# Performance work log

Measured on AMD Instinct MI355X. Metric: run time of the kernel, lower is better.

The kernel has to match this reference:

```python
import jax, jax.numpy as jnp
import numpy as np

V = 59      # input features (mimic_59f)
H = 128     # hidden size
B = 2048
T = 96

def _uniform(key, shape, fan_in):
    s = 1.0 / np.sqrt(fan_in)
    return jax.random.uniform(key, shape, jnp.float32, -s, s)

def setup_inputs() -> dict:
    key = jax.random.key(0)
    ks = jax.random.split(key, 20)
    x = jax.random.normal(ks[0], (B, T, V), jnp.float32)
    mask = (jax.random.uniform(ks[1], (B, T, V)) < 0.8).astype(jnp.float32)
    deltas = jax.random.uniform(ks[2], (B, T, V), jnp.float32)
    return {
        'x': x, 'mask': mask, 'deltas': deltas,
        # temp_decay_h: Decay(V -> H)
        'Wdh': _uniform(ks[3], (H, V), V), 'bdh': _uniform(ks[4], (H,), V),
        # temp_decay_x: Decay(V -> V, diag)
        'Wdx': _uniform(ks[5], (V, V), V), 'bdx': _uniform(ks[6], (V,), V),
        # hist: Linear(H -> V)
        'Wh': _uniform(ks[7], (V, H), H), 'bh': _uniform(ks[8], (V,), H),
        'Wf': _uniform(ks[9], (V, V), V), 'bf': _uniform(ks[10], (V,), V),
        # weight_combine: Linear(2V -> V)
        'Wc': _uniform(ks[11], (V, 2 * V), 2 * V), 'bc': _uniform(ks[12], (V,), 2 * V),
        # GRUCell(2V -> H): gates ordered [r, z, n]
        'Wih': _uniform(ks[13], (3 * H, 2 * V), 2 * V), 'Whh': _uniform(ks[14], (3 * H, H), H),
        'bih': _uniform(ks[15], (3 * H,), H), 'bhh': _uniform(ks[16], (3 * H,), H),
    }


def reference(x, mask, deltas, Wdh, bdh, Wdx, bdx, Wh, bh, Wf, bf, Wc, bc, Wih, Whh, bih, bhh):
    Bb, Tt, Vv = x.shape
    eye = jnp.eye(Vv, dtype=x.dtype)
    Wdx_d = Wdx * eye            # diagonal decay
    Wf_m = Wf * (1.0 - eye)

    def step(h, inp):
        x_t, m_t, d_t = inp                                  # each [B, V]
        gamma_h = jnp.exp(-jax.nn.relu(d_t @ Wdh.T + bdh))   # [B, H]
        h = h * gamma_h
        x_h = h @ Wh.T + bh                                   # [B, V]
        x_r = m_t * x_t + (1.0 - m_t) * x_h
        xu = x_r @ Wf_m.T + bf
        gamma_x = jnp.exp(-jax.nn.relu(d_t @ Wdx_d.T + bdx))
        beta = jnp.concatenate([gamma_x, m_t], axis=1) @ Wc.T + bc
        x_comb = beta * xu + (1.0 - beta) * x_h
        loss_t = jnp.sum(jnp.abs(x_t - x_comb) * m_t) / (jnp.sum(m_t) + 1e-5)
        x_imp_t = m_t * x_t + (1.0 - m_t) * x_comb
        inp_t = jnp.concatenate([x_imp_t, m_t], axis=1)       # [B, 2V]
        gi = inp_t @ Wih.T + bih                              # [B, 3H]
        gh = h @ Whh.T + bhh
        ir, iz, inn = jnp.split(gi, 3, axis=1)
        hr, hz, hn = jnp.split(gh, 3, axis=1)
        r = jax.nn.sigmoid(ir + hr)
        z = jax.nn.sigmoid(iz + hz)
        n = jnp.tanh(inn + r * hn)
        h_new = (1.0 - z) * n + z * h
        return h_new, (x_imp_t, h_new, loss_t)

    xs = (jnp.swapaxes(x, 0, 1), jnp.swapaxes(mask, 0, 1), jnp.swapaxes(deltas, 0, 1))
    h0 = jnp.zeros((Bb, Wdh.shape[0]), x.dtype)
    _, (x_imp, Hiddens, losses) = jax.lax.scan(step, h0, xs)
    return (jnp.swapaxes(x_imp, 0, 1),      # imputation [B, T, V]
            jnp.sum(losses),                 # xloss scalar
            jnp.swapaxes(Hiddens, 0, 1))     # hidden_state [B, T, H]
```

## Files before the change

kernel.cpp:

```cpp
#include <hip/hip_runtime.h>
#include <hip/hip_bf16.h>
#include <math.h>

#define VF 59
#define HF 128
#define BB 2048
#define TT 96
#define MR 16
#define NBLK (BB / MR)
#define NTH 512

typedef __attribute__((ext_vector_type(8))) short short8;
typedef __attribute__((ext_vector_type(4))) float f32x4;

#define MFMA(a, b, c) __builtin_amdgcn_mfma_f32_16x16x32_bf16((a), (b), (c), 0, 0, 0)

#define WF_INV   0
#define WF_ACC   96
#define WF_DWDX  192
#define WF_END   256
#define U_B1  (WF_END * 2)
#define U_B2  (U_B1 + 8192)
#define U_B3  (U_B2 + 8192)
#define U_B4  (U_B3 + 4096)
#define U_B5  (U_B4 + 8192)
#define U_B6  (U_B5 + 49152)

#define LOSS_IDX (BB * TT * VF)
#define OFF_HID  (BB * TT * VF + 1)

#define S_AD    0
#define S_AH    1024
#define S_AGM   3072
#define S_AIM0  5120
#define S_AIM1  7168
#define S_AXR   9216
#define F_SX    5120
#define F_SM    6080
#define F_SB    7040
#define F_RED   8064
#define F_IDT   8072
#define F_TOT   8168

__device__ __forceinline__ ushort f2bf(float f) {
    __hip_bfloat16 h = __float2bfloat16(f);
    return *reinterpret_cast<ushort*>(&h);
}
__device__ __forceinline__ float sigm(float v) { return 1.f / (1.f + __expf(-v)); }
__device__ __forceinline__ float tanh_f(float v) {
    float c = fminf(fmaxf(v, -15.f), 15.f);
    float e = __expf(-2.f * c);
    return (1.f - e) / (1.f + e);
}
__device__ __forceinline__ int fragIdx(int row, int col) {
    return ((col >> 5) * 64 + ((col >> 3) & 3) * 16 + row) * 8 + (col & 7);
}
__device__ __forceinline__ int betaIdx(int m, int col) {
    return m * 64 + ((col + 4 * m) & 63);
}

__device__ __forceinline__ void block_sync() {
    asm volatile("s_waitcnt lgkmcnt(0)" ::: "memory");
    __builtin_amdgcn_s_barrier();
    asm volatile("" ::: "memory");
}

__global__ __launch_bounds__(128) void prep_zero(float* __restrict__ ws, float* __restrict__ loss_ptr) {
    int tid = threadIdx.x;
    if (tid < TT) ws[WF_ACC + tid] = 0.f;
    if (tid == 96) loss_ptr[0] = 0.f;
}

#define PA_R 128
__global__ __launch_bounds__(256) void prep_acc(const float* __restrict__ mask, float* __restrict__ ws) {
    __shared__ float buf[PA_R * VF];
    __shared__ float acc[TT];
    int tid = threadIdx.x;
    if (tid < TT) acc[tid] = 0.f;
    const float4* src = (const float4*)(mask + (size_t)blockIdx.x * (PA_R * VF));
    float4* dst = (float4*)buf;
    #pragma unroll
    for (int i = 0; i < 8; ++i) {
        int idx = tid + i * 256;
        if (idx < PA_R * VF / 4) dst[idx] = src[idx];
    }
    __syncthreads();
    if (tid < PA_R) {
        float s = 0.f;
        #pragma unroll
        for (int v = 0; v < VF; ++v) s += buf[tid * VF + v];
        int t = (blockIdx.x * PA_R + tid) % TT;
        atomicAdd(&acc[t], s);
    }
    __syncthreads();
    if (tid < TT) atomicAdd(&ws[WF_ACC + tid], acc[tid]);
}

__device__ void packB(const float* __restrict__ W, int G, int K, int tiles, int KS,
                      int zdiag, ushort* __restrict__ dst, int gtid, int gstride) {
    int total = tiles * KS * 512;
    for (int idx = gtid; idx < total; idx += gstride) {
        int j  = idx & 7;
        int l  = (idx >> 3) & 63;
        int tk = idx >> 9;
        int ks = tk % KS;
        int tile = tk / KS;
        int g = tile * 16 + (l & 15);
        int k = ks * 32 + ((l >> 4) << 3) + j;
        float v = 0.f;
        if (g < G && k < K) v = W[g * K + k];
        if (zdiag && g == k) v = 0.f;
        dst[idx] = f2bf(v);
    }
}

__global__ __launch_bounds__(256) void prep_pack(
    const float* __restrict__ Wdh, const float* __restrict__ Wdx,
    const float* __restrict__ Wh,  const float* __restrict__ Wf,
    const float* __restrict__ Wc,  const float* __restrict__ Wih,
    const float* __restrict__ Whh, float* __restrict__ ws)
{
    int blk = blockIdx.x, tid = threadIdx.x;
    if (blk == 64) {
        if (tid < TT) ws[WF_INV + tid] = 1.f / (ws[WF_ACC + tid] + 1e-5f);
        if (tid < VF) ws[WF_DWDX + tid] = Wdx[tid * VF + tid];
        return;
    }
    ushort* wsu = (ushort*)ws;
    int gtid = blk * 256 + tid;
    int gstride = 64 * 256;
    packB(Wdh, HF,     VF,     8,  2, 0, wsu + U_B1, gtid, gstride);
    packB(Wh,  VF,     HF,     4,  4, 0, wsu + U_B2, gtid, gstride);
    packB(Wf,  VF,     VF,     4,  2, 1, wsu + U_B3, gtid, gstride);
    packB(Wc,  VF,     2*VF,   4,  4, 0, wsu + U_B4, gtid, gstride);
    packB(Wih, 3*HF,   2*VF,   24, 4, 0, wsu + U_B5, gtid, gstride);
    packB(Whh, 3*HF,   HF,     24, 4, 0, wsu + U_B6, gtid, gstride);
}

__global__ __launch_bounds__(NTH, 2) void rits_main(
    const float* __restrict__ x, const float* __restrict__ mask, const float* __restrict__ deltas,
    const float* __restrict__ bdh, const float* __restrict__ bdx, const float* __restrict__ bh,
    const float* __restrict__ bf,  const float* __restrict__ bc,
    const float* __restrict__ bih, const float* __restrict__ bhh,
    const float* __restrict__ ws, float* __restrict__ out)
{
    __shared__ __align__(16) float smf[F_TOT];
    ushort* smu = (ushort*)smf;

    const int tid  = threadIdx.x;
    const int lane = tid & 63;
    const int w    = tid >> 6;
    const int ln15 = lane & 15;
    const int quad = lane >> 4;
    const int b0   = blockIdx.x * MR;

    const ushort* wsu = (const ushort*)ws;
    const short8* B1 = (const short8*)(wsu + U_B1);
    const short8* B2 = (const short8*)(wsu + U_B2);
    const short8* B3 = (const short8*)(wsu + U_B3);
    const short8* B4 = (const short8*)(wsu + U_B4);
    const short8* B5 = (const short8*)(wsu + U_B5);
    const short8* B6 = (const short8*)(wsu + U_B6);

    short8 wB1[2];
    #pragma unroll
    for (int i = 0; i < 2; ++i) wB1[i] = B1[(w * 2 + i) * 64 + lane];
    short8 wB24[4];
    #pragma unroll
    for (int ks = 0; ks < 4; ++ks)
        wB24[ks] = (w < 4) ? B2[(w * 4 + ks) * 64 + lane]
                           : B4[((w - 4) * 4 + ks) * 64 + lane];
    short8 wB3[2];
    #pragma unroll
    for (int i = 0; i < 2; ++i) wB3[i] = B3[(((w < 4) ? w : (w - 4)) * 2 + i) * 64 + lane];
    short8 wB5[12], wB6[12];
    #pragma unroll
    for (int tt = 0; tt < 3; ++tt)
        #pragma unroll
        for (int ks = 0; ks < 4; ++ks) {
            wB5[tt * 4 + ks] = B5[((w + tt * 8) * 4 + ks) * 64 + lane];
            wB6[tt * 4 + ks] = B6[((w + tt * 8) * 4 + ks) * 64 + lane];
        }

    const int jH = w * 16 + ln15;
    const float c_bdh = bdh[jH];
    const float c_br  = bih[jH]       + bhh[jH];
    const float c_bz  = bih[jH + 128] + bhh[jH + 128];
    const float c_bin = bih[jH + 256];
    const float c_bhn = bhh[jH + 256];
    const int vC = (w < 4 ? w : w - 4) * 16 + ln15;
    const float c_bh = (vC < VF) ? bh[vC] : 0.f;
    const float c_bf = (vC < VF) ? bf[vC] : 0.f;
    const float c_bc = (vC < VF) ? bc[vC] : 0.f;

    const int q  = tid & 255;
    const int lr = q >> 4;
    const int lc = q & 15;
    const size_t rowbase = (size_t)(b0 + lr) * (TT * VF);
    const float* px = x + rowbase;
    const float* pm = mask + rowbase;
    const float* pd = deltas + rowbase;
    float wdx4[4], bdx4[4];
    #pragma unroll
    for (int k = 0; k < 4; ++k) {
        int v = lc + 16 * k;
        wdx4[k] = (v < VF) ? ws[WF_DWDX + v] : 0.f;
        bdx4[k] = (v < VF) ? bdx[v] : 0.f;
    }

    float hreg[4] = {0.f, 0.f, 0.f, 0.f};

    for (int i = tid; i < F_TOT; i += NTH) smf[i] = 0.f;
    __syncthreads();

    if (tid < TT) smf[F_IDT + tid] = ws[WF_INV + tid];
    if (w >= 4) {
        #pragma unroll
        for (int k = 0; k < 4; ++k) {
            int v = lc + 16 * k;
            if (v < VF) {
                float xv = px[v], mv = pm[v], dv = pd[v];
                smf[F_SX + lr * 60 + v] = xv;
                smf[F_SM + lr * 60 + v] = mv;
                ushort mb = f2bf(mv);
                smu[S_AGM  + fragIdx(lr, 59 + v)] = mb;
                smu[S_AIM0 + fragIdx(lr, 59 + v)] = mb;
                float gx = __expf(-fmaxf(fmaf(dv, wdx4[k], bdx4[k]), 0.f));
                smu[S_AGM + fragIdx(lr, v)] = f2bf(gx);
            }
        }
    }
    __syncthreads();

    float loss_acc = 0.f;

    for (int t = 0; t < TT; ++t) {
        float pxv[4], pmv[4], pdv[4];
        if (w >= 4 && t + 1 < TT) {
            const size_t toff = (size_t)(t + 1) * VF;
            #pragma unroll
            for (int k = 0; k < 4; ++k) {
                int v = lc + 16 * k;
                if (v < VF) { pxv[k] = px[toff + v]; pmv[k] = pm[toff + v]; pdv[k] = pd[toff + v]; }
            }
        }

        short8 ah[4];
        #pragma unroll
        for (int ks = 0; ks < 4; ++ks)
            ah[ks] = *(const short8*)(smu + S_AH + (ks * 64 + lane) * 8);
        f32x4 gHa[3];
        #pragma unroll
        for (int tt = 0; tt < 3; ++tt) gHa[tt] = (f32x4){0.f, 0.f, 0.f, 0.f};
        float xh[4], mmv[4];
        if (w < 4) {
            f32x4 acc = {0.f, 0.f, 0.f, 0.f};
            #pragma unroll
            for (int ks = 0; ks < 4; ++ks) acc = MFMA(ah[ks], wB24[ks], acc);
            #pragma unroll
            for (int tt = 0; tt < 3; ++tt)
                #pragma unroll
                for (int ks = 0; ks < 4; ++ks) gHa[tt] = MFMA(ah[ks], wB6[tt * 4 + ks], gHa[tt]);
            if (vC < VF) {
                #pragma unroll
                for (int i = 0; i < 4; ++i) {
                    int m = quad * 4 + i;
                    xh[i] = acc[i] + c_bh;
                    float mm = smf[F_SM + m * 60 + vC];
                    mmv[i] = mm;
                    float xr = fmaf(mm, smf[F_SX + m * 60 + vC], (1.f - mm) * xh[i]);
                    smu[S_AXR + fragIdx(m, vC)] = f2bf(xr);
                }
            }
        } else {
            short8 ag[4];
            #pragma unroll
            for (int ks = 0; ks < 4; ++ks)
                ag[ks] = *(const short8*)(smu + S_AGM + (ks * 64 + lane) * 8);
            f32x4 acc = {0.f, 0.f, 0.f, 0.f};
            #pragma unroll
            for (int ks = 0; ks < 4; ++ks) acc = MFMA(ag[ks], wB24[ks], acc);
            #pragma unroll
            for (int tt = 0; tt < 3; ++tt)
                #pragma unroll
                for (int ks = 0; ks < 4; ++ks) gHa[tt] = MFMA(ah[ks], wB6[tt * 4 + ks], gHa[tt]);
            if (vC < VF) {
                #pragma unroll
                for (int i = 0; i < 4; ++i) {
                    int m = quad * 4 + i;
                    smf[F_SB + betaIdx(m, vC)] = acc[i] + c_bc;
                }
            }
        }
        block_sync();

        if (w < 4) {
            short8 a0 = *(const short8*)(smu + S_AXR + (0 * 64 + lane) * 8);
            short8 a1 = *(const short8*)(smu + S_AXR + (1 * 64 + lane) * 8);
            f32x4 acc = {0.f, 0.f, 0.f, 0.f};
            acc = MFMA(a0, wB3[0], acc);
            acc = MFMA(a1, wB3[1], acc);
            if (vC < VF) {
                const float idt = smf[F_IDT + t];
                const int aimW = S_AIM0 + (t & 1) * 2048;
                #pragma unroll
                for (int i = 0; i < 4; ++i) {
                    int m = quad * 4 + i;
                    float xu   = acc[i] + c_bf;
                    float beta = smf[F_SB + betaIdx(m, vC)];
                    float xc   = beta * xu + (1.f - beta) * xh[i];
                    float mm   = mmv[i];
                    float xv   = smf[F_SX + m * 60 + vC];
                    loss_acc += fabsf(xv - xc) * mm * idt;
                    float xi = fmaf(mm, xv, (1.f - mm) * xc);
                    out[(size_t)(b0 + m) * (TT * VF) + (size_t)t * VF + vC] = xi;
                    smu[aimW + fragIdx(m, vC)] = f2bf(xi);
                }
            }
        } else if (t + 1 < TT) {
            #pragma unroll
            for (int k = 0; k < 4; ++k) {
                int v = lc + 16 * k;
                if (v < VF) {
                    smu[S_AD + fragIdx(lr, v)] = f2bf(pdv[k]);
                    float gx = __expf(-fmaxf(fmaf(pdv[k], wdx4[k], bdx4[k]), 0.f));
                    smu[S_AGM + fragIdx(lr, v)] = f2bf(gx);
                }
            }
        }
        block_sync();

        {
            const int aimR = S_AIM0 + (t & 1) * 2048;
            short8 ai[4];
            #pragma unroll
            for (int ks = 0; ks < 4; ++ks)
                ai[ks] = *(const short8*)(smu + aimR + (ks * 64 + lane) * 8);
            f32x4 gI[3];
            #pragma unroll
            for (int tt = 0; tt < 3; ++tt) gI[tt] = (f32x4){0.f, 0.f, 0.f, 0.f};
            #pragma unroll
            for (int tt = 0; tt < 3; ++tt)
                #pragma unroll
                for (int ks = 0; ks < 4; ++ks) gI[tt] = MFMA(ai[ks], wB5[tt * 4 + ks], gI[tt]);
            float gdec[4] = {0.f, 0.f, 0.f, 0.f};
            if (t + 1 < TT) {
                short8 d0 = *(const short8*)(smu + S_AD + (0 * 64 + lane) * 8);
                short8 d1 = *(const short8*)(smu + S_AD + (1 * 64 + lane) * 8);
                f32x4 gacc = {0.f, 0.f, 0.f, 0.f};
                gacc = MFMA(d0, wB1[0], gacc);
                gacc = MFMA(d1, wB1[1], gacc);
                #pragma unroll
                for (int i = 0; i < 4; ++i)
                    gdec[i] = __expf(-fmaxf(gacc[i] + c_bdh, 0.f));
            }
            #pragma unroll
            for (int i = 0; i < 4; ++i) {
                int m = quad * 4 + i;
                float r_ = sigm(gI[0][i] + gHa[0][i] + c_br);
                float z_ = sigm(gI[1][i] + gHa[1][i] + c_bz);
                float hn = gHa[2][i] + c_bhn;
                float n_ = tanh_f(fmaf(r_, hn, gI[2][i] + c_bin));
                float hnew = fmaf(z_, hreg[i] - n_, n_);
                out[OFF_HID + (size_t)(b0 + m) * (TT * HF) + (size_t)t * HF + jH] = hnew;
                float hd = hnew * gdec[i];
                hreg[i] = hd;
                if (t + 1 < TT) smu[S_AH + fragIdx(m, jH)] = f2bf(hd);
            }
        }
        if (w >= 4 && t + 1 < TT) {
            const int aimN = S_AIM0 + ((t + 1) & 1) * 2048;
            #pragma unroll
            for (int k = 0; k < 4; ++k) {
                int v = lc + 16 * k;
                if (v < VF) {
                    smf[F_SX + lr * 60 + v] = pxv[k];
                    smf[F_SM + lr * 60 + v] = pmv[k];
                    ushort mb = f2bf(pmv[k]);
                    smu[S_AGM + fragIdx(lr, 59 + v)] = mb;
                    smu[aimN  + fragIdx(lr, 59 + v)] = mb;
                }
            }
        }
        block_sync();
    }

    __syncthreads();
    float vsum = loss_acc;
    for (int off = 32; off > 0; off >>= 1) vsum += __shfl_down(vsum, off);
    if (lane == 0) smf[F_RED + w] = vsum;
    __syncthreads();
    if (tid == 0) {
        float s = 0.f;
        #pragma unroll
        for (int i = 0; i < 8; ++i) s += smf[F_RED + i];
        atomicAdd(out + LOSS_IDX, s);
    }
}

extern "C" void kernel_launch(void* const* d_in, const int* in_sizes, int n_in,
                              void* d_out, int out_size, void* d_ws, size_t ws_size,
                              hipStream_t stream) {
    const float* x      = (const float*)d_in[0];
    const float* mask   = (const float*)d_in[1];
    const float* deltas = (const float*)d_in[2];
    const float* Wdh    = (const float*)d_in[3];
    const float* bdh    = (const float*)d_in[4];
    const float* Wdx    = (const float*)d_in[5];
    const float* bdx    = (const float*)d_in[6];
    const float* Wh     = (const float*)d_in[7];
    const float* bh     = (const float*)d_in[8];
    const float* Wf     = (const float*)d_in[9];
    const float* bf     = (const float*)d_in[10];
    const float* Wc     = (const float*)d_in[11];
    const float* bc     = (const float*)d_in[12];
    const float* Wih    = (const float*)d_in[13];
    const float* Whh    = (const float*)d_in[14];
    const float* bih    = (const float*)d_in[15];
    const float* bhh    = (const float*)d_in[16];
    float* out = (float*)d_out;
    float* ws  = (float*)d_ws;

    prep_zero<<<1, 128, 0, stream>>>(ws, out + LOSS_IDX);
    prep_acc<<<(BB * TT) / PA_R, 256, 0, stream>>>(mask, ws);
    prep_pack<<<65, 256, 0, stream>>>(Wdh, Wdx, Wh, Wf, Wc, Wih, Whh, ws);
    rits_main<<<NBLK, NTH, 0, stream>>>(x, mask, deltas, bdh, bdx, bh, bf, bc,
                                        bih, bhh, ws, out);
}
```

Baseline: 527.2 us.

## Fuse per-timestep mask sums into main kernel and finalize loss separately

Removes the separate prep_acc pass that reread the whole mask tensor to compute per-timestep normalizers. The main kernel now accumulates mask sums and raw loss numerators per timestep in shared memory, using wave reductions and shared atomics, then atomically adds them into the workspace. A small trailing kernel divides and sums them into the loss. It also switches to pointer-increment addressing and explicit waves-per-EU attributes, and adds extra shared atomics and reductions inside the time loop.

```diff
diff --git a/kernel.cpp b/kernel.cpp
--- a/kernel.cpp
+++ b/kernel.cpp
@@ -15,8 +15,8 @@
 
 #define MFMA(a, b, c) __builtin_amdgcn_mfma_f32_16x16x32_bf16((a), (b), (c), 0, 0, 0)
 
-#define WF_INV   0
-#define WF_ACC   96
+#define WF_MS    0
+#define WF_RAW   96
 #define WF_DWDX  192
 #define WF_END   256
 #define U_B1  (WF_END * 2)
@@ -38,9 +38,9 @@
 #define F_SX    5120
 #define F_SM    6080
 #define F_SB    7040
-#define F_RED   8064
-#define F_IDT   8072
-#define F_TOT   8168
+#define F_MS    8064
+#define F_LT    8160
+#define F_TOT   8256
 
 __device__ __forceinline__ ushort f2bf(float f) {
     __hip_bfloat16 h = __float2bfloat16(f);
@@ -58,6 +58,11 @@
 __device__ __forceinline__ int betaIdx(int m, int col) {
     return m * 64 + ((col + 4 * m) & 63);
 }
+__device__ __forceinline__ float wave_red(float v) {
+    #pragma unroll
+    for (int o = 32; o > 0; o >>= 1) v += __shfl_down(v, o);
+    return v;
+}
 
 __device__ __forceinline__ void block_sync() {
     asm volatile("s_waitcnt lgkmcnt(0)" ::: "memory");
@@ -65,35 +70,9 @@
     asm volatile("" ::: "memory");
 }
 
-__global__ __launch_bounds__(128) void prep_zero(float* __restrict__ ws, float* __restrict__ loss_ptr) {
+__global__ __launch_bounds__(192) void prep_zero(float* __restrict__ ws) {
     int tid = threadIdx.x;
-    if (tid < TT) ws[WF_ACC + tid] = 0.f;
-    if (tid == 96) loss_ptr[0] = 0.f;
-}
-
-#define PA_R 128
-__global__ __launch_bounds__(256) void prep_acc(const float* __restrict__ mask, float* __restrict__ ws) {
-    __shared__ float buf[PA_R * VF];
-    __shared__ float acc[TT];
-    int tid = threadIdx.x;
-    if (tid < TT) acc[tid] = 0.f;
-    const float4* src = (const float4*)(mask + (size_t)blockIdx.x * (PA_R * VF));
-    float4* dst = (float4*)buf;
-    #pragma unroll
-    for (int i = 0; i < 8; ++i) {
-        int idx = tid + i * 256;
-        if (idx < PA_R * VF / 4) dst[idx] = src[idx];
-    }
-    __syncthreads();
-    if (tid < PA_R) {
-        float s = 0.f;
-        #pragma unroll
-        for (int v = 0; v < VF; ++v) s += buf[tid * VF + v];
-        int t = (blockIdx.x * PA_R + tid) % TT;
-        atomicAdd(&acc[t], s);
-    }
-    __syncthreads();
-    if (tid < TT) atomicAdd(&ws[WF_ACC + tid], acc[tid]);
+    if (tid < 192) ws[tid] = 0.f;
 }
 
 __device__ void packB(const float* __restrict__ W, int G, int K, int tiles, int KS,
@@ -122,7 +101,6 @@
 {
     int blk = blockIdx.x, tid = threadIdx.x;
     if (blk == 64) {
-        if (tid < TT) ws[WF_INV + tid] = 1.f / (ws[WF_ACC + tid] + 1e-5f);
         if (tid < VF) ws[WF_DWDX + tid] = Wdx[tid * VF + tid];
         return;
     }
@@ -137,7 +115,18 @@
     packB(Whh, 3*HF,   HF,     24, 4, 0, wsu + U_B6, gtid, gstride);
 }
 
-__global__ __launch_bounds__(NTH, 2) void rits_main(
+__global__ __launch_bounds__(128) void loss_fin(const float* __restrict__ ws, float* __restrict__ out) {
+    __shared__ float red[2];
+    int tid = threadIdx.x;
+    float v = (tid < TT) ? ws[WF_RAW + tid] / (ws[WF_MS + tid] + 1e-5f) : 0.f;
+    v = wave_red(v);
+    if ((tid & 63) == 0) red[tid >> 6] = v;
+    __syncthreads();
+    if (tid == 0) out[LOSS_IDX] = red[0] + red[1];
+}
+
+__global__ __attribute__((amdgpu_flat_work_group_size(NTH, NTH), amdgpu_waves_per_eu(2, 2)))
+void rits_main(
     const float* __restrict__ x, const float* __restrict__ mask, const float* __restrict__ deltas,
     const float* __restrict__ bdh, const float* __restrict__ bdx, const float* __restrict__ bh,
     const float* __restrict__ bf,  const float* __restrict__ bc,
@@ -213,8 +202,8 @@
     for (int i = tid; i < F_TOT; i += NTH) smf[i] = 0.f;
     __syncthreads();
 
-    if (tid < TT) smf[F_IDT + tid] = ws[WF_INV + tid];
     if (w >= 4) {
+        float msum0 = 0.f;
         #pragma unroll
         for (int k = 0; k < 4; ++k) {
             int v = lc + 16 * k;
@@ -227,21 +216,25 @@
                 smu[S_AIM0 + fragIdx(lr, 59 + v)] = mb;
                 float gx = __expf(-fmaxf(fmaf(dv, wdx4[k], bdx4[k]), 0.f));
                 smu[S_AGM + fragIdx(lr, v)] = f2bf(gx);
-            }
-        }
+                msum0 += mv;
+            }
+        }
+        float ms = wave_red(msum0);
+        if (lane == 0) atomicAdd(&smf[F_MS + 0], ms);
     }
     __syncthreads();
 
-    float loss_acc = 0.f;
+    const float* pxt = px + VF;
+    const float* pmt = pm + VF;
+    const float* pdt = pd + VF;
 
     for (int t = 0; t < TT; ++t) {
         float pxv[4], pmv[4], pdv[4];
         if (w >= 4 && t + 1 < TT) {
-            const size_t toff = (size_t)(t + 1) * VF;
             #pragma unroll
             for (int k = 0; k < 4; ++k) {
                 int v = lc + 16 * k;
-                if (v < VF) { pxv[k] = px[toff + v]; pmv[k] = pm[toff + v]; pdv[k] = pd[toff + v]; }
+                if (v < VF) { pxv[k] = pxt[v]; pmv[k] = pmt[v]; pdv[k] = pdt[v]; }
             }
         }
 
@@ -300,8 +293,8 @@
             f32x4 acc = {0.f, 0.f, 0.f, 0.f};
             acc = MFMA(a0, wB3[0], acc);
             acc = MFMA(a1, wB3[1], acc);
+            float lsum = 0.f;
             if (vC < VF) {
-                const float idt = smf[F_IDT + t];
                 const int aimW = S_AIM0 + (t & 1) * 2048;
                 #pragma unroll
                 for (int i = 0; i < 4; ++i) {
@@ -311,12 +304,14 @@
                     float xc   = beta * xu + (1.f - beta) * xh[i];
                     float mm   = mmv[i];
                     float xv   = smf[F_SX + m * 60 + vC];
-                    loss_acc += fabsf(xv - xc) * mm * idt;
+                    lsum += fabsf(xv - xc) * mm;
                     float xi = fmaf(mm, xv, (1.f - mm) * xc);
                     out[(size_t)(b0 + m) * (TT * VF) + (size_t)t * VF + vC] = xi;
                     smu[aimW + fragIdx(m, vC)] = f2bf(xi);
                 }
             }
+            float ls = wave_red(lsum);
+            if (lane == 0) atomicAdd(&smf[F_LT + t], ls);
         } else if (t + 1 < TT) {
             #pragma unroll
             for (int k = 0; k < 4; ++k) {
@@ -370,6 +365,7 @@
         }
         if (w >= 4 && t + 1 < TT) {
             const int aimN = S_AIM0 + ((t + 1) & 1) * 2048;
+            float msum = 0.f;
             #pragma unroll
             for (int k = 0; k < 4; ++k) {
                 int v = lc + 16 * k;
@@ -379,23 +375,20 @@
                     ushort mb = f2bf(pmv[k]);
                     smu[S_AGM + fragIdx(lr, 59 + v)] = mb;
                     smu[aimN  + fragIdx(lr, 59 + v)] = mb;
+                    msum += pmv[k];
                 }
             }
-        }
+            float ms = wave_red(msum);
+            if (lane == 0) atomicAdd(&smf[F_MS + t + 1], ms);
+        }
+        pxt += VF; pmt += VF; pdt += VF;
         block_sync();
     }
 
     __syncthreads();
-    float vsum = loss_acc;
-    for (int off = 32; off > 0; off >>= 1) vsum += __shfl_down(vsum, off);
-    if (lane == 0) smf[F_RED + w] = vsum;
-    __syncthreads();
-    if (tid == 0) {
-        float s = 0.f;
-        #pragma unroll
-        for (int i = 0; i < 8; ++i) s += smf[F_RED + i];
-        atomicAdd(out + LOSS_IDX, s);
-    }
+    float* wsw = const_cast<float*>(ws);
+    if (tid < TT) atomicAdd(wsw + WF_MS + tid, smf[F_MS + tid]);
+    else if (tid < 2 * TT) atomicAdd(wsw + WF_RAW + (tid - TT), smf[F_LT + (tid - TT)]);
 }
 
 extern "C" void kernel_launch(void* const* d_in, const int* in_sizes, int n_in,
@@ -421,9 +414,9 @@
     float* out = (float*)d_out;
     float* ws  = (float*)d_ws;
 
-    prep_zero<<<1, 128, 0, stream>>>(ws, out + LOSS_IDX);
-    prep_acc<<<(BB * TT) / PA_R, 256, 0, stream>>>(mask, ws);
+    prep_zero<<<1, 192, 0, stream>>>(ws);
     prep_pack<<<65, 256, 0, stream>>>(Wdh, Wdx, Wh, Wf, Wc, Wih, Whh, ws);
     rits_main<<<NBLK, NTH, 0, stream>>>(x, mask, deltas, bdh, bdx, bh, bf, bc,
                                         bih, bhh, ws, out);
-}
+    loss_fin<<<1, 128, 0, stream>>>(ws, out);
+}
```

After: 579.0 us. 1.1x slower.
